# Performance work log

Measured on AMD Instinct MI355X. Metric: run time of the kernel, lower is better.

The kernel has to match this reference:

```python
import jax, jax.numpy as jnp
import numpy as np

B, S, D = 2, 4096, 768


def setup_inputs() -> dict:
    key = jax.random.key(0)
    kx, kq, kk, kv, ko = jax.random.split(key, 5)
    x = jax.random.normal(kx, (B, S, D), dtype=jnp.float32)
    # nn.Linear weights are [out, in]; init std=0.01 per _init_weights
    Wq = 0.01 * jax.random.normal(kq, (D, D), dtype=jnp.float32)
    Wk = 0.01 * jax.random.normal(kk, (D, D), dtype=jnp.float32)
    Wv = 0.01 * jax.random.normal(kv, (D, D), dtype=jnp.float32)
    Wo = 0.01 * jax.random.normal(ko, (D, D), dtype=jnp.float32)
    return {"x": x, "Wq": Wq, "Wk": Wk, "Wv": Wv, "Wo": Wo}


def reference(x, Wq, Wk, Wv, Wo):
    # nn.Linear: y = x @ W.T
    q = jnp.einsum('bsd,ed->bse', x, Wq) * 0.1
    k = jnp.einsum('bsd,ed->bse', x, Wk) * 0.1
    v = jnp.einsum('bsd,ed->bse', x, Wv)
    attn = jnp.einsum('bqd,bkd->bqk', q, k) * 0.1          # [B,S,S]
    attn = attn * attn + attn                               # polynomial "softmax"
    attn_out = jnp.einsum('bqk,bkd->bqd', attn, v)
    out = jnp.einsum('bsd,ed->bse', attn_out, Wo) * 0.1
    return out
```

## Files before the change

### kernel.cpp

```cpp
#include <hip/hip_runtime.h>
#include <hip/hip_bf16.h>


typedef __attribute__((ext_vector_type(8))) __bf16 bf16x8;
typedef __attribute__((ext_vector_type(4))) float f32x4;
typedef __attribute__((ext_vector_type(4))) float float4v;
typedef __attribute__((ext_vector_type(8))) unsigned short u16x8;
typedef __attribute__((ext_vector_type(4))) unsigned short u16x4;

__device__ inline unsigned short f2bf(float f) {
    union { float f; unsigned int u; } v; v.f = f;
    unsigned int r = v.u + 0x7FFFu + ((v.u >> 16) & 1u);
    return (unsigned short)(r >> 16);
}

__global__ __launch_bounds__(256) void cvt_f32_bf16(const float* __restrict__ in,
                                                    unsigned short* __restrict__ out,
                                                    int n4) {
    int i = blockIdx.x * 256 + threadIdx.x;
    if (i < n4) {
        float4v v = *(const float4v*)(in + (size_t)i * 4);
        u16x4 h;
        h[0] = f2bf(v[0]); h[1] = f2bf(v[1]); h[2] = f2bf(v[2]); h[3] = f2bf(v[3]);
        *(u16x4*)(out + (size_t)i * 4) = h;
    }
}

__global__ __launch_bounds__(256) void cvt3_f32_bf16(const float* __restrict__ a,
                                                     const float* __restrict__ b,
                                                     const float* __restrict__ c,
                                                     unsigned short* __restrict__ oa,
                                                     unsigned short* __restrict__ ob,
                                                     unsigned short* __restrict__ oc,
                                                     int n4) {
    const float* in = blockIdx.y == 0 ? a : blockIdx.y == 1 ? b : c;
    unsigned short* out = blockIdx.y == 0 ? oa : blockIdx.y == 1 ? ob : oc;
    int i = blockIdx.x * 256 + threadIdx.x;
    if (i < n4) {
        float4v v = *(const float4v*)(in + (size_t)i * 4);
        u16x4 h;
        h[0] = f2bf(v[0]); h[1] = f2bf(v[1]); h[2] = f2bf(v[2]); h[3] = f2bf(v[3]);
        *(u16x4*)(out + (size_t)i * 4) = h;
    }
}

__global__ __launch_bounds__(256) void cvt_t_f32_bf16(const float* __restrict__ in,
                                                      unsigned short* __restrict__ outT,
                                                      int n) {
    __shared__ float tile[32][33];
    int c0 = blockIdx.x * 32, r0 = blockIdx.y * 32;
    int tx = threadIdx.x & 31, ty = threadIdx.x >> 5;
#pragma unroll
    for (int j = 0; j < 4; ++j)
        tile[ty + 8 * j][tx] = in[(size_t)(r0 + ty + 8 * j) * n + c0 + tx];
    __syncthreads();
#pragma unroll
    for (int j = 0; j < 4; ++j)
        outT[(size_t)(c0 + ty + 8 * j) * n + r0 + tx] = f2bf(tile[tx][ty + 8 * j]);
}

__device__ inline void gld16(const void* g, void* l) {
    __builtin_amdgcn_global_load_lds(
        (const __attribute__((address_space(1))) unsigned int*)g,
        (__attribute__((address_space(3))) unsigned int*)l, 16, 0, 0);
}

template <int TN, bool POLY, typename TO>
__device__ __forceinline__ void gemm_core(const unsigned short* __restrict__ A,
                                          const unsigned short* __restrict__ B,
                                          TO* __restrict__ C,
                                          int K, int lda, int ldb, int ldc,
                                          float scale, int bx, int by,
                                          unsigned short* As, unsigned short* Bs) {
    constexpr int NR = TN / 32;
    const int t = threadIdx.x, l = t & 63, wid = t >> 6;
    const int m0 = by * 128, n0 = bx * TN;
    const int wr = wid >> 1, wc = wid & 1;
    const int lrow = l & 15, kslot = l >> 4;

    const int ce = (((l & 7) ^ ((l >> 3) & 7)) << 3);
    const unsigned short* Ag = A + (size_t)(m0 + wid * 8 + (l >> 3)) * lda + ce;
    const unsigned short* Bg = B + (size_t)(n0 + wid * 8 + (l >> 3)) * ldb + ce;

    f32x4 acc[4][NR] = {};

    for (int k0 = 0; k0 < K; k0 += 64) {
#pragma unroll
        for (int s = 0; s < 4; ++s)
            gld16(Ag + (size_t)(s * 32) * lda + k0, As + s * 2048 + wid * 512);
#pragma unroll
        for (int s = 0; s < TN / 32; ++s)
            gld16(Bg + (size_t)(s * 32) * ldb + k0, Bs + s * 2048 + wid * 512);
        __syncthreads();

        bf16x8 af[4][2], bfr[NR][2];
#pragma unroll
        for (int kk = 0; kk < 2; ++kk) {
#pragma unroll
            for (int mi = 0; mi < 4; ++mi) {
                int r = wr * 64 + mi * 16 + lrow;
                int j = (kk * 4 + kslot) ^ (r & 7);
                u16x8 v = *(const u16x8*)(As + r * 64 + j * 8);
                af[mi][kk] = __builtin_bit_cast(bf16x8, v);
            }
#pragma unroll
            for (int ni = 0; ni < NR; ++ni) {
                int r = wc * (TN / 2) + ni * 16 + lrow;
                int j = (kk * 4 + kslot) ^ (r & 7);
                u16x8 v = *(const u16x8*)(Bs + r * 64 + j * 8);
                bfr[ni][kk] = __builtin_bit_cast(bf16x8, v);
            }
        }
#pragma unroll
        for (int kk = 0; kk < 2; ++kk)
#pragma unroll
            for (int mi = 0; mi < 4; ++mi)
#pragma unroll
                for (int ni = 0; ni < NR; ++ni)
                    acc[mi][ni] = __builtin_amdgcn_mfma_f32_16x16x32_bf16(
                        af[mi][kk], bfr[ni][kk], acc[mi][ni], 0, 0, 0);
        __syncthreads();
    }

#pragma unroll
    for (int mi = 0; mi < 4; ++mi) {
        int rbase = m0 + wr * 64 + mi * 16 + kslot * 4;
#pragma unroll
        for (int ni = 0; ni < NR; ++ni) {
            int col = n0 + wc * (TN / 2) + ni * 16 + lrow;
#pragma unroll
            for (int r = 0; r < 4; ++r) {
                float v = acc[mi][ni][r] * scale;
                if constexpr (POLY) v = v * v + v;
                if constexpr (sizeof(TO) == 2)
                    C[(size_t)(rbase + r) * ldc + col] = f2bf(v);
                else
                    C[(size_t)(rbase + r) * ldc + col] = v;
            }
        }
    }
}

template <int TN, bool POLY, typename TO, bool SWZ>
__global__ __launch_bounds__(256) void gemm_bt(const unsigned short* __restrict__ A,
                                               const unsigned short* __restrict__ B,
                                               TO* __restrict__ C,
                                               int K, int lda, int ldb, int ldc,
                                               float scale,
                                               long long szA, long long szB, long long szC) {
    __shared__ __align__(16) unsigned short As[128 * 64];
    __shared__ __align__(16) unsigned short Bs[TN * 64];
    int bx = blockIdx.x, by = blockIdx.y;
    if constexpr (SWZ) {
        int gx = gridDim.x;
        int nwg = gx * gridDim.y;
        int chunk = nwg >> 3;
        int flat = by * gx + bx;
        int f2 = (flat & 7) * chunk + (flat >> 3);
        bx = f2 % gx; by = f2 / gx;
    }
    const size_t z = blockIdx.z;
    gemm_core<TN, POLY, TO>(A + z * szA, B + z * szB, C + z * szC,
                            K, lda, ldb, ldc, scale, bx, by, As, Bs);
}

__global__ __launch_bounds__(256) void gemm_proj2(const unsigned short* __restrict__ xb,
                                                  const unsigned short* __restrict__ Wqkb,
                                                  unsigned short* __restrict__ QK,
                                                  const unsigned short* __restrict__ Wovb,
                                                  unsigned short* __restrict__ VWt) {
    __shared__ __align__(16) unsigned short As[128 * 64];
    __shared__ __align__(16) unsigned short Bs[128 * 64];
    int bid = blockIdx.x;
    if (bid < 768) {
        gemm_core<128, false, unsigned short>(xb, Wqkb, QK, 768, 768, 768, 1536, 1.0f,
                                              bid % 12, bid / 12, As, Bs);
    } else {
        int r = bid - 768;
        gemm_core<128, false, unsigned short>(Wovb, xb, VWt, 768, 768, 768, 8192, 1.0f,
                                              r % 64, r / 64, As, Bs);
    }
}

extern "C" void kernel_launch(void* const* d_in, const int* in_sizes, int n_in,
                              void* d_out, int out_size, void* d_ws, size_t ws_size,
                              hipStream_t stream) {
    const float* x  = (const float*)d_in[0];
    const float* Wq = (const float*)d_in[1];
    const float* Wk = (const float*)d_in[2];
    const float* Wv = (const float*)d_in[3];
    const float* Wo = (const float*)d_in[4];
    float* out = (float*)d_out;

    const int BS = 8192, S = 4096, D = 768, D2 = 1536;
    const long long SD = (long long)S * D, SS = (long long)S * S;
    unsigned short* ws = (unsigned short*)d_ws;
    size_t o = 0;
    unsigned short* QK   = ws + o; o += (size_t)BS * D2;
    unsigned short* VWt  = ws + o; o += (size_t)BS * D;
    unsigned short* Wqkb = ws + o; o += (size_t)D2 * D;
    unsigned short* Wob  = ws + o; o += (size_t)D * D;
    unsigned short* WvT  = ws + o; o += (size_t)D * D;
    unsigned short* Wovb = ws + o; o += (size_t)D * D;
    unsigned short* xb   = ws + o;
    unsigned short* P    = xb;
    const size_t oxb = o;

    const bool batched = ws_size >= (oxb + 2ull * SS) * 2ull;

    dim3 blk(256);
    cvt_f32_bf16<<<dim3(BS * D / 1024), blk, 0, stream>>>(x, xb, BS * D / 4);
    cvt3_f32_bf16<<<dim3(D * D / 1024, 3), blk, 0, stream>>>(
        Wq, Wk, Wo, Wqkb, Wqkb + (size_t)D * D, Wob, D * D / 4);
    cvt_t_f32_bf16<<<dim3(D / 32, D / 32), blk, 0, stream>>>(Wv, WvT, D);

    gemm_bt<128, false, unsigned short, false><<<dim3(6, 6, 1), blk, 0, stream>>>(
        Wob, WvT, Wovb, D, D, D, D, 1.0f, 0, 0, 0);
    gemm_proj2<<<dim3(1152), blk, 0, stream>>>(xb, Wqkb, QK, Wovb, VWt);

    if (batched) {
        gemm_bt<128, true, unsigned short, false><<<dim3(S / 128, S / 128, 2), blk, 0, stream>>>(
            QK, QK + D, P, D, D2, D2, S, 1e-3f,
            (long long)S * D2, (long long)S * D2, SS);
        gemm_bt<64, false, float, true><<<dim3(D / 64, S / 128, 2), blk, 0, stream>>>(
            P, VWt, out, S, S, BS, D, 0.1f, SS, (long long)S, SD);
    } else {
        for (int b = 0; b < 2; ++b) {
            gemm_bt<128, true, unsigned short, false><<<dim3(S / 128, S / 128, 1), blk, 0, stream>>>(
                QK + (size_t)b * S * D2, QK + (size_t)b * S * D2 + D, P,
                D, D2, D2, S, 1e-3f, 0, 0, 0);
            gemm_bt<64, false, float, true><<<dim3(D / 64, S / 128, 1), blk, 0, stream>>>(
                P, VWt + (size_t)b * S, out + (size_t)b * SD, S, S, BS, D, 0.1f, 0, 0, 0);
        }
    }
}
```

Before: 283.8 us.

## Add 256x256-tile 8-wave QK^T GEMM with double-buffered LDS and swizzle

Replaces the 128x128 QK^T scoring GEMM with a dedicated kernel using 256x256 output tiles, 512 threads (8 waves, each 128x64), and 128KB of dynamic LDS. Tiles are double-buffered so the global loads for the next K slice overlap the current MFMAs, and an XOR swizzle avoids bank conflicts. Barriers are interleaved with s_setprio around the MFMA bursts. The larger tile gives more reuse per loaded byte, at the cost of high register and LDS pressure, fewer blocks (256 for the batch), and uncoalesced scalar bf16 stores in the epilogue.

Measured after the change: 269.9 us. 1.05x faster.

```diff
diff --git a/kernel.cpp b/kernel.cpp
--- a/kernel.cpp
+++ b/kernel.cpp
@@ -182,6 +182,113 @@
     }
 }
 
+template <bool POLY>
+__global__ __launch_bounds__(512, 2) void gemm_qkt8(const unsigned short* __restrict__ A,
+                                                    const unsigned short* __restrict__ B,
+                                                    unsigned short* __restrict__ C,
+                                                    int K, int lda, int ldb, int ldc,
+                                                    float scale,
+                                                    long long szA, long long szB, long long szC) {
+    extern __shared__ __align__(16) unsigned short lds[];
+    const int t = threadIdx.x, l = t & 63, w = t >> 6;
+    const int wm = w >> 2, wn = w & 3;
+    const int m0 = blockIdx.y * 256, n0 = blockIdx.x * 256;
+    const size_t z = blockIdx.z;
+    A += z * szA; B += z * szB; C += z * szC;
+    const int lrow = l & 15, kslot = l >> 4;
+    const int jc = lrow & 7;
+    const int arow = (wm * 128 + lrow) * 64;
+    const int brow = (wn * 64 + lrow) * 64;
+
+    const int ce = (((l & 7) ^ ((l >> 3) & 7)) << 3);
+    const unsigned short* Ag = A + (size_t)(m0 + w * 32 + (l >> 3)) * lda + ce;
+    const unsigned short* Bg = B + (size_t)(n0 + w * 32 + (l >> 3)) * ldb + ce;
+
+    f32x4 acc[8][4] = {};
+    const int NP = K >> 6;
+
+#pragma unroll
+    for (int j = 0; j < 4; ++j) {
+        gld16(Ag + (size_t)(j * 8) * lda, &lds[w * 2048 + j * 512]);
+        gld16(Bg + (size_t)(j * 8) * ldb, &lds[32768 + w * 2048 + j * 512]);
+    }
+    asm volatile("s_waitcnt vmcnt(0)" ::: "memory");
+    __builtin_amdgcn_s_barrier();
+
+    for (int P = 0; P < NP; ++P) {
+        const unsigned short* as = &lds[(P & 1) * 16384];
+        const unsigned short* bs = &lds[32768 + (P & 1) * 16384];
+        unsigned short* asn = &lds[((P + 1) & 1) * 16384];
+        unsigned short* bsn = &lds[32768 + ((P + 1) & 1) * 16384];
+        const bool st = (P + 1) < NP;
+        const unsigned short* Agn = Ag + ((P + 1) << 6);
+        const unsigned short* Bgn = Bg + ((P + 1) << 6);
+
+#pragma unroll
+        for (int sg = 0; sg < 2; ++sg) {
+            const int jb = ((sg * 4 + kslot) ^ jc) * 8;
+            bf16x8 a[4], b[4];
+#pragma unroll
+            for (int i = 0; i < 4; ++i) {
+                u16x8 v = *(const u16x8*)(as + arow + i * 1024 + jb);
+                a[i] = __builtin_bit_cast(bf16x8, v);
+            }
+#pragma unroll
+            for (int i = 0; i < 4; ++i) {
+                u16x8 v = *(const u16x8*)(bs + brow + i * 1024 + jb);
+                b[i] = __builtin_bit_cast(bf16x8, v);
+            }
+            if (sg == 0 && st) {
+#pragma unroll
+                for (int j = 0; j < 4; ++j) {
+                    gld16(Agn + (size_t)(j * 8) * lda, asn + w * 2048 + j * 512);
+                    gld16(Bgn + (size_t)(j * 8) * ldb, bsn + w * 2048 + j * 512);
+                }
+            }
+            __builtin_amdgcn_s_barrier();
+            __builtin_amdgcn_s_setprio(1);
+#pragma unroll
+            for (int i = 0; i < 4; ++i)
+#pragma unroll
+                for (int n = 0; n < 4; ++n)
+                    acc[i][n] = __builtin_amdgcn_mfma_f32_16x16x32_bf16(a[i], b[n], acc[i][n], 0, 0, 0);
+            __builtin_amdgcn_s_setprio(0);
+            __builtin_amdgcn_s_barrier();
+#pragma unroll
+            for (int i = 0; i < 4; ++i) {
+                u16x8 v = *(const u16x8*)(as + arow + 4096 + i * 1024 + jb);
+                a[i] = __builtin_bit_cast(bf16x8, v);
+            }
+            __builtin_amdgcn_s_barrier();
+            __builtin_amdgcn_s_setprio(1);
+#pragma unroll
+            for (int i = 0; i < 4; ++i)
+#pragma unroll
+                for (int n = 0; n < 4; ++n)
+                    acc[4 + i][n] = __builtin_amdgcn_mfma_f32_16x16x32_bf16(a[i], b[n], acc[4 + i][n], 0, 0, 0);
+            __builtin_amdgcn_s_setprio(0);
+            if (sg == 1)
+                asm volatile("s_waitcnt vmcnt(0)" ::: "memory");
+            __builtin_amdgcn_s_barrier();
+        }
+    }
+
+#pragma unroll
+    for (int mi = 0; mi < 8; ++mi) {
+        int row = m0 + wm * 128 + mi * 16 + kslot * 4;
+#pragma unroll
+        for (int n = 0; n < 4; ++n) {
+            int col = n0 + wn * 64 + n * 16 + lrow;
+#pragma unroll
+            for (int rr = 0; rr < 4; ++rr) {
+                float v = acc[mi][n][rr] * scale;
+                if constexpr (POLY) v = v * v + v;
+                C[(size_t)(row + rr) * ldc + col] = f2bf(v);
+            }
+        }
+    }
+}
+
 extern "C" void kernel_launch(void* const* d_in, const int* in_sizes, int n_in,
                               void* d_out, int out_size, void* d_ws, size_t ws_size,
                               hipStream_t stream) {
@@ -208,6 +315,13 @@
 
     const bool batched = ws_size >= (oxb + 2ull * SS) * 2ull;
 
+    static int lds_ok = 0;
+    if (!lds_ok) {
+        hipFuncSetAttribute((const void*)gemm_qkt8<true>,
+                            hipFuncAttributeMaxDynamicSharedMemorySize, 131072);
+        lds_ok = 1;
+    }
+
     dim3 blk(256);
     cvt_f32_bf16<<<dim3(BS * D / 1024), blk, 0, stream>>>(x, xb, BS * D / 4);
     cvt3_f32_bf16<<<dim3(D * D / 1024, 3), blk, 0, stream>>>(
@@ -219,14 +333,14 @@
     gemm_proj2<<<dim3(1152), blk, 0, stream>>>(xb, Wqkb, QK, Wovb, VWt);
 
     if (batched) {
-        gemm_bt<128, true, unsigned short, false><<<dim3(S / 128, S / 128, 2), blk, 0, stream>>>(
+        gemm_qkt8<true><<<dim3(S / 256, S / 256, 2), dim3(512), 131072, stream>>>(
             QK, QK + D, P, D, D2, D2, S, 1e-3f,
             (long long)S * D2, (long long)S * D2, SS);
         gemm_bt<64, false, float, true><<<dim3(D / 64, S / 128, 2), blk, 0, stream>>>(
             P, VWt, out, S, S, BS, D, 0.1f, SS, (long long)S, SD);
     } else {
         for (int b = 0; b < 2; ++b) {
-            gemm_bt<128, true, unsigned short, false><<<dim3(S / 128, S / 128, 1), blk, 0, stream>>>(
+            gemm_qkt8<true><<<dim3(S / 256, S / 256, 1), dim3(512), 131072, stream>>>(
                 QK + (size_t)b * S * D2, QK + (size_t)b * S * D2 + D, P,
                 D, D2, D2, S, 1e-3f, 0, 0, 0);
             gemm_bt<64, false, float, true><<<dim3(D / 64, S / 128, 1), blk, 0, stream>>>(
```
